# Kernel tuning notes

Measured on AMD Instinct MI355X. Metric: run time of the kernel, lower is better.

Reference implementation:

```python
import jax, jax.numpy as jnp
import numpy as np


def setup_inputs() -> dict:
    key = jax.random.key(0)
    ks = jax.random.split(key, 6)
    B, S, I, H = 8, 4096, 512, 512
    scale = 1.0 / np.sqrt(I)
    return {
        "x": jax.random.normal(ks[0], (B, S, I), dtype=jnp.float32),
        "h_0": jax.random.normal(ks[1], (B, H), dtype=jnp.float32),
        "W_z": jax.random.normal(ks[2], (H, I), dtype=jnp.float32) * scale,
        "b_z": jax.random.normal(ks[3], (H,), dtype=jnp.float32) * scale,
        "W_h": jax.random.normal(ks[4], (H, I), dtype=jnp.float32) * scale,
        "b_h": jax.random.normal(ks[5], (H,), dtype=jnp.float32) * scale,
    }


def reference(x, h_0, W_z, b_z, W_h, b_h):
    # Gate and candidate projections (dense GEMMs over all timesteps at once)
    z = jax.nn.sigmoid(jnp.einsum("bsi,hi->bsh", x, W_z) + b_z)  # [B,S,H]
    h_tilde = jnp.einsum("bsi,hi->bsh", x, W_h) + b_h            # [B,S,H]

    # Linear recurrence h_t = a_t * h_{t-1} + b_t with a = 1-z, b = z*h_tilde.
    # Parallel associative scan over time; h_0 folded in as element 0 (a=1, b=h_0).
    a = jnp.concatenate([jnp.ones_like(h_0)[:, None, :], 1.0 - z], axis=1)     # [B,S+1,H]
    b = jnp.concatenate([h_0[:, None, :], z * h_tilde], axis=1)                # [B,S+1,H]

    def combine(c1, c2):
        a1, b1 = c1
        a2, b2 = c2
        return a1 * a2, a2 * b1 + b2

    _, h = jax.lax.associative_scan(combine, (a, b), axis=1)
    return h[:, 1:, :]  # drop the h_0 slot -> [B,S,H]
```

## Files before the change

kernel.cpp:

```cpp
#include <hip/hip_runtime.h>
#include <hip/hip_bf16.h>
#include <stdint.h>


typedef __attribute__((ext_vector_type(8))) short short8;
typedef __attribute__((ext_vector_type(4))) float f32x4;

#define AS1 __attribute__((address_space(1)))
#define AS3 __attribute__((address_space(3)))

__device__ inline void gload_lds16(const void* g, void* l) {
  __builtin_amdgcn_global_load_lds((AS1 uint32_t*)(g), (AS3 uint32_t*)(l), 16, 0, 0);
}

__device__ inline ushort f2bf(float f) {
  union { __hip_bfloat16 h; ushort u; } v;
  v.h = __float2bfloat16(f);
  return v.u;
}

__global__ void cvt_all(const float* __restrict__ x,
                        const float* __restrict__ wz,
                        const float* __restrict__ wh,
                        ushort* __restrict__ xb,
                        ushort* __restrict__ wzb,
                        ushort* __restrict__ whb) {
  int i = blockIdx.x * 256 + threadIdx.x;
  for (; i < 4325376; i += 2048 * 256) {
    const float* s; ushort* d; int j;
    if (i < 4194304)      { s = x;  d = xb;  j = i; }
    else if (i < 4259840) { s = wz; d = wzb; j = i - 4194304; }
    else                  { s = wh; d = whb; j = i - 4259840; }
    float4 v = reinterpret_cast<const float4*>(s)[j];
    ushort4 o = make_ushort4(f2bf(v.x), f2bf(v.y), f2bf(v.z), f2bf(v.w));
    reinterpret_cast<ushort4*>(d)[j] = o;
  }
}

__global__ __launch_bounds__(256, 2) void gemm_gate(
    const ushort* __restrict__ xb,
    const ushort* __restrict__ wzb,
    const ushort* __restrict__ whb,
    const float* __restrict__ b_z,
    const float* __restrict__ b_h,
    uint* __restrict__ ab,
    float2* __restrict__ ABc)
{
  __shared__ __align__(16) char smem[73728];

  const int t  = threadIdx.x;
  const int w  = t >> 6;
  const int l  = t & 63;
  const int lm = l & 15;
  const int lk = l >> 4;
  const int wm = w >> 1, wn = w & 1;
  const int bid  = blockIdx.x;
  const int tile = (bid & 7) * 128 + (bid >> 3);
  const int bx = tile >> 2;
  const int by = tile & 3;
  const int m0 = bx * 128;
  const int n0 = by * 128;

  const int srow = t >> 2;
  const int ssl  = t & 3;

  f32x4 acc[2][4][4];
  #pragma unroll
  for (int q = 0; q < 2; ++q)
    #pragma unroll
    for (int m = 0; m < 4; ++m)
      #pragma unroll
      for (int n = 0; n < 4; ++n)
        acc[q][m][n] = (f32x4){0.f, 0.f, 0.f, 0.f};

  auto stage = [&](int sel, int kt) {
    char* base = smem + sel * 24576;
    const int k0 = kt * 32;
    #pragma unroll
    for (int j = 0; j < 2; ++j) {
      int row = j * 64 + srow;
      int gs  = ssl ^ ((row >> 1) & 3);
      gload_lds16(xb + (size_t)(m0 + row) * 512 + k0 + gs * 8,
                  base + j * 4096 + w * 1024);
      gload_lds16(wzb + (size_t)(n0 + row) * 512 + k0 + gs * 8,
                  base + 8192 + j * 4096 + w * 1024);
      gload_lds16(whb + (size_t)(n0 + row) * 512 + k0 + gs * 8,
                  base + 16384 + j * 4096 + w * 1024);
    }
  };

  stage(0, 0);
  stage(1, 1);

  #pragma unroll
  for (int kt = 0; kt < 16; ++kt) {
    const int sel = kt % 3;
    if (kt < 14) {
      stage((kt + 2) % 3, kt + 2);
      asm volatile("s_waitcnt vmcnt(12)" ::: "memory");
    } else if (kt == 14) {
      asm volatile("s_waitcnt vmcnt(6)" ::: "memory");
    } else {
      asm volatile("s_waitcnt vmcnt(0)" ::: "memory");
    }
    __builtin_amdgcn_s_barrier();

    const char* base = smem + sel * 24576;
    short8 af[4], bfz[4], bfh[4];
    #pragma unroll
    for (int m = 0; m < 4; ++m) {
      int row = wm * 64 + m * 16 + lm;
      af[m] = *(const short8*)(base + row * 64 + ((lk ^ ((row >> 1) & 3)) << 4));
    }
    #pragma unroll
    for (int n = 0; n < 4; ++n) {
      int row = wn * 64 + n * 16 + lm;
      int so  = ((lk ^ ((row >> 1) & 3)) << 4);
      bfz[n] = *(const short8*)(base + 8192  + row * 64 + so);
      bfh[n] = *(const short8*)(base + 16384 + row * 64 + so);
    }
    __builtin_amdgcn_s_setprio(1);
    #pragma unroll
    for (int m = 0; m < 4; ++m)
      #pragma unroll
      for (int n = 0; n < 4; ++n) {
        acc[0][m][n] = __builtin_amdgcn_mfma_f32_16x16x32_bf16(af[m], bfz[n], acc[0][m][n], 0, 0, 0);
        acc[1][m][n] = __builtin_amdgcn_mfma_f32_16x16x32_bf16(af[m], bfh[n], acc[1][m][n], 0, 0, 0);
      }
    __builtin_amdgcn_s_setprio(0);
    __builtin_amdgcn_s_barrier();
  }

  #pragma unroll
  for (int n = 0; n < 4; ++n) {
    const int col = n0 + wn * 64 + n * 16 + lm;
    const float bzn = b_z[col];
    const float bhn = b_h[col];
    float av[4][4], bv[4][4];
    #pragma unroll
    for (int m = 0; m < 4; ++m) {
      #pragma unroll
      for (int j = 0; j < 4; ++j) {
        size_t grow = (size_t)(m0 + wm * 64 + m * 16 + lk * 4 + j);
        float uz = acc[0][m][n][j] + bzn;
        float uh = acc[1][m][n][j] + bhn;
        float z  = 1.f / (1.f + __expf(-uz));
        float a  = 1.f - z;
        float bb = z * uh;
        av[m][j] = a;
        bv[m][j] = bb;
        ab[grow * 512 + n0 + wn * 64 + n * 16 + lm] =
            (uint)f2bf(a) | ((uint)f2bf(bb) << 16);
      }
    }
    #pragma unroll
    for (int cb = 0; cb < 2; ++cb) {
      float At[2], Bt[2];
      #pragma unroll
      for (int mm = 0; mm < 2; ++mm) {
        float A = 1.f, Bv = 0.f;
        #pragma unroll
        for (int j = 0; j < 4; ++j) {
          float a = av[2 * cb + mm][j];
          float b = bv[2 * cb + mm][j];
          A  = a * A;
          Bv = a * Bv + b;
        }
        float Ag = 1.f, Bg = 0.f;
        #pragma unroll
        for (int q = 0; q < 4; ++q) {
          float Aq = __shfl(A,  lm + 16 * q);
          float Bq = __shfl(Bv, lm + 16 * q);
          Ag = Aq * Ag;
          Bg = Aq * Bg + Bq;
        }
        At[mm] = Ag;
        Bt[mm] = Bg;
      }
      float Achunk = At[1] * At[0];
      float Bchunk = At[1] * Bt[0] + Bt[1];
      if (lk == 0) {
        int bidx = bx >> 5;
        int c    = (bx & 31) * 4 + wm * 2 + cb;
        ABc[((size_t)bidx * 512 + col) * 128 + c] = make_float2(Achunk, Bchunk);
      }
    }
  }
}

__global__ __launch_bounds__(256) void chunk_scan(
    const float2* __restrict__ ABc,
    const float* __restrict__ h0,
    float* __restrict__ Hinit)
{
  __shared__ float sm[128][4];
  const int w = threadIdx.x >> 6, l = threadIdx.x & 63;
  const int b   = blockIdx.x >> 7;
  const int h0g = (blockIdx.x & 127) * 4;
  const int h   = h0g + w;

  const float2* base = ABc + ((size_t)b * 512 + h) * 128;
  float2 s1 = base[l];
  float2 s2 = base[64 + l];

  float A1 = s1.x, B1 = s1.y;
  #pragma unroll
  for (int d = 1; d < 64; d <<= 1) {
    float uA = __shfl_up(A1, d);
    float uB = __shfl_up(B1, d);
    if (l >= d) { B1 = A1 * uB + B1; A1 = A1 * uA; }
  }
  float A2 = s2.x, B2 = s2.y;
  #pragma unroll
  for (int d = 1; d < 64; d <<= 1) {
    float uA = __shfl_up(A2, d);
    float uB = __shfl_up(B2, d);
    if (l >= d) { B2 = A2 * uB + B2; A2 = A2 * uA; }
  }
  float PA = __shfl(A1, 63), PB = __shfl(B1, 63);
  float FA = A2 * PA;
  float FB = A2 * PB + B2;

  float e1A = __shfl_up(A1, 1), e1B = __shfl_up(B1, 1);
  if (l == 0) { e1A = 1.f; e1B = 0.f; }
  float e2A = __shfl_up(FA, 1), e2B = __shfl_up(FB, 1);
  if (l == 0) { e2A = PA; e2B = PB; }

  float h0v = h0[b * 512 + h];
  sm[l][w]      = e1A * h0v + e1B;
  sm[64 + l][w] = e2A * h0v + e2B;
  __syncthreads();

  const int tt = threadIdx.x;
  if (tt < 128) {
    float4 v = *(const float4*)sm[tt];
    *(float4*)(Hinit + ((size_t)b * 128 + tt) * 512 + h0g) = v;
  }
}

__global__ __launch_bounds__(256) void scan_write(
    const uint* __restrict__ ab,
    const float* __restrict__ Hinit,
    float* __restrict__ out)
{
  int tid = blockIdx.x * 256 + threadIdx.x;
  int cg = tid & 127;
  int c  = (tid >> 7) & 127;
  int b  = tid >> 14;
  const uint4* p = reinterpret_cast<const uint4*>(ab + ((size_t)(b * 4096 + c * 32)) * 512) + cg;
  float4 hv = *reinterpret_cast<const float4*>(Hinit + ((size_t)b * 128 + c) * 512 + cg * 4);
  float4* po = reinterpret_cast<float4*>(out + ((size_t)(b * 4096 + c * 32)) * 512) + cg;
  #pragma unroll 4
  for (int t = 0; t < 32; ++t) {
    uint4 u = p[(size_t)t * 128];
    hv.x = __uint_as_float(u.x << 16) * hv.x + __uint_as_float(u.x & 0xffff0000u);
    hv.y = __uint_as_float(u.y << 16) * hv.y + __uint_as_float(u.y & 0xffff0000u);
    hv.z = __uint_as_float(u.z << 16) * hv.z + __uint_as_float(u.z & 0xffff0000u);
    hv.w = __uint_as_float(u.w << 16) * hv.w + __uint_as_float(u.w & 0xffff0000u);
    po[(size_t)t * 128] = hv;
  }
}

extern "C" void kernel_launch(void* const* d_in, const int* in_sizes, int n_in,
                              void* d_out, int out_size, void* d_ws, size_t ws_size,
                              hipStream_t stream) {
  const float* x   = (const float*)d_in[0];
  const float* h0  = (const float*)d_in[1];
  const float* W_z = (const float*)d_in[2];
  const float* b_z = (const float*)d_in[3];
  const float* W_h = (const float*)d_in[4];
  const float* b_h = (const float*)d_in[5];
  float* out = (float*)d_out;

  char* ws = (char*)d_ws;
  ushort* xb    = (ushort*)(ws);
  ushort* wzb   = (ushort*)(ws + 33554432);
  ushort* whb   = (ushort*)(ws + 34078720);
  uint*   ab    = (uint*)  (ws + 34603008);
  float2* ABc   = (float2*)(ws + 101711872);
  float*  Hinit = (float*) (ws + 105906176);

  cvt_all<<<2048, 256, 0, stream>>>(x, W_z, W_h, xb, wzb, whb);
  gemm_gate<<<1024, 256, 0, stream>>>(xb, wzb, whb, b_z, b_h, ab, ABc);
  chunk_scan<<<1024, 256, 0, stream>>>(ABc, h0, Hinit);
  scan_write<<<512, 256, 0, stream>>>(ab, Hinit, out);
}
```

Measured before the change: 94.55 us.

## Fuse fp32-to-bf16 conversion of x into GEMM LDS staging

Drops the separate pass that converted the whole x tensor to bf16 in workspace. The GEMM now streams fp32 x straight into LDS and converts each fragment to bf16 in registers before the MFMAs. Only the weights are still converted up front. This saves a full read and write of x (64 MB fp32 in, 32 MB bf16 out), but doubles x's LDS footprint, so the pipeline drops from triple to double buffering and conversion ALU work lands on the GEMM critical path.

Result: faster. 88.03 us (-6.9%).

```diff
diff --git a/kernel.cpp b/kernel.cpp
--- a/kernel.cpp
+++ b/kernel.cpp
@@ -19,26 +19,19 @@
   return v.u;
 }
 
-__global__ void cvt_all(const float* __restrict__ x,
-                        const float* __restrict__ wz,
-                        const float* __restrict__ wh,
-                        ushort* __restrict__ xb,
-                        ushort* __restrict__ wzb,
-                        ushort* __restrict__ whb) {
+__global__ void cvt_w(const float* __restrict__ wz, const float* __restrict__ wh,
+                      ushort* __restrict__ wzb, ushort* __restrict__ whb) {
   int i = blockIdx.x * 256 + threadIdx.x;
-  for (; i < 4325376; i += 2048 * 256) {
-    const float* s; ushort* d; int j;
-    if (i < 4194304)      { s = x;  d = xb;  j = i; }
-    else if (i < 4259840) { s = wz; d = wzb; j = i - 4194304; }
-    else                  { s = wh; d = whb; j = i - 4259840; }
-    float4 v = reinterpret_cast<const float4*>(s)[j];
-    ushort4 o = make_ushort4(f2bf(v.x), f2bf(v.y), f2bf(v.z), f2bf(v.w));
-    reinterpret_cast<ushort4*>(d)[j] = o;
-  }
+  float4 a = reinterpret_cast<const float4*>(wz)[i];
+  reinterpret_cast<ushort4*>(wzb)[i] =
+      make_ushort4(f2bf(a.x), f2bf(a.y), f2bf(a.z), f2bf(a.w));
+  float4 b = reinterpret_cast<const float4*>(wh)[i];
+  reinterpret_cast<ushort4*>(whb)[i] =
+      make_ushort4(f2bf(b.x), f2bf(b.y), f2bf(b.z), f2bf(b.w));
 }
 
 __global__ __launch_bounds__(256, 2) void gemm_gate(
-    const ushort* __restrict__ xb,
+    const float* __restrict__ x,
     const ushort* __restrict__ wzb,
     const ushort* __restrict__ whb,
     const float* __restrict__ b_z,
@@ -46,7 +39,7 @@
     uint* __restrict__ ab,
     float2* __restrict__ ABc)
 {
-  __shared__ __align__(16) char smem[73728];
+  __shared__ __align__(16) char smem[65536];
 
   const int t  = threadIdx.x;
   const int w  = t >> 6;
@@ -74,50 +67,58 @@
         acc[q][m][n] = (f32x4){0.f, 0.f, 0.f, 0.f};
 
   auto stage = [&](int sel, int kt) {
-    char* base = smem + sel * 24576;
+    char* base = smem + sel * 32768;
     const int k0 = kt * 32;
     #pragma unroll
     for (int j = 0; j < 2; ++j) {
-      int row = j * 64 + srow;
-      int gs  = ssl ^ ((row >> 1) & 3);
-      gload_lds16(xb + (size_t)(m0 + row) * 512 + k0 + gs * 8,
-                  base + j * 4096 + w * 1024);
+      int row  = j * 64 + srow;
+      int sw   = (row >> 1) & 3;
+      int qlog = ssl ^ sw;
+      const float* xs = x + (size_t)(m0 + row) * 512 + k0 + qlog * 8;
+      gload_lds16(xs,     base +        j * 4096 + w * 1024);
+      gload_lds16(xs + 4, base + 8192 + j * 4096 + w * 1024);
+      int gs = ssl ^ sw;
       gload_lds16(wzb + (size_t)(n0 + row) * 512 + k0 + gs * 8,
-                  base + 8192 + j * 4096 + w * 1024);
+                  base + 16384 + j * 4096 + w * 1024);
       gload_lds16(whb + (size_t)(n0 + row) * 512 + k0 + gs * 8,
-                  base + 16384 + j * 4096 + w * 1024);
+                  base + 24576 + j * 4096 + w * 1024);
     }
   };
 
   stage(0, 0);
-  stage(1, 1);
 
   #pragma unroll
   for (int kt = 0; kt < 16; ++kt) {
-    const int sel = kt % 3;
-    if (kt < 14) {
-      stage((kt + 2) % 3, kt + 2);
-      asm volatile("s_waitcnt vmcnt(12)" ::: "memory");
-    } else if (kt == 14) {
-      asm volatile("s_waitcnt vmcnt(6)" ::: "memory");
+    const int sel = kt & 1;
+    if (kt < 15) {
+      stage(sel ^ 1, kt + 1);
+      asm volatile("s_waitcnt vmcnt(8)" ::: "memory");
     } else {
       asm volatile("s_waitcnt vmcnt(0)" ::: "memory");
     }
     __builtin_amdgcn_s_barrier();
 
-    const char* base = smem + sel * 24576;
+    const char* base = smem + sel * 32768;
     short8 af[4], bfz[4], bfh[4];
     #pragma unroll
     for (int m = 0; m < 4; ++m) {
       int row = wm * 64 + m * 16 + lm;
-      af[m] = *(const short8*)(base + row * 64 + ((lk ^ ((row >> 1) & 3)) << 4));
+      int so  = ((lk ^ ((row >> 1) & 3)) << 4);
+      f32x4 lo = *(const f32x4*)(base +        row * 64 + so);
+      f32x4 hi = *(const f32x4*)(base + 8192 + row * 64 + so);
+      short8 v;
+      v[0] = (short)f2bf(lo[0]); v[1] = (short)f2bf(lo[1]);
+      v[2] = (short)f2bf(lo[2]); v[3] = (short)f2bf(lo[3]);
+      v[4] = (short)f2bf(hi[0]); v[5] = (short)f2bf(hi[1]);
+      v[6] = (short)f2bf(hi[2]); v[7] = (short)f2bf(hi[3]);
+      af[m] = v;
     }
     #pragma unroll
     for (int n = 0; n < 4; ++n) {
       int row = wn * 64 + n * 16 + lm;
       int so  = ((lk ^ ((row >> 1) & 3)) << 4);
-      bfz[n] = *(const short8*)(base + 8192  + row * 64 + so);
-      bfh[n] = *(const short8*)(base + 16384 + row * 64 + so);
+      bfz[n] = *(const short8*)(base + 16384 + row * 64 + so);
+      bfh[n] = *(const short8*)(base + 24576 + row * 64 + so);
     }
     __builtin_amdgcn_s_setprio(1);
     #pragma unroll
@@ -149,8 +150,7 @@
         float bb = z * uh;
         av[m][j] = a;
         bv[m][j] = bb;
-        ab[grow * 512 + n0 + wn * 64 + n * 16 + lm] =
-            (uint)f2bf(a) | ((uint)f2bf(bb) << 16);
+        ab[grow * 512 + col] = (uint)f2bf(a) | ((uint)f2bf(bb) << 16);
       }
     }
     #pragma unroll
@@ -273,15 +273,14 @@
   float* out = (float*)d_out;
 
   char* ws = (char*)d_ws;
-  ushort* xb    = (ushort*)(ws);
-  ushort* wzb   = (ushort*)(ws + 33554432);
-  ushort* whb   = (ushort*)(ws + 34078720);
-  uint*   ab    = (uint*)  (ws + 34603008);
-  float2* ABc   = (float2*)(ws + 101711872);
-  float*  Hinit = (float*) (ws + 105906176);
-
-  cvt_all<<<2048, 256, 0, stream>>>(x, W_z, W_h, xb, wzb, whb);
-  gemm_gate<<<1024, 256, 0, stream>>>(xb, wzb, whb, b_z, b_h, ab, ABc);
+  ushort* wzb   = (ushort*)(ws);
+  ushort* whb   = (ushort*)(ws + 524288);
+  uint*   ab    = (uint*)  (ws + 1048576);
+  float2* ABc   = (float2*)(ws + 68157440);
+  float*  Hinit = (float*) (ws + 72351744);
+
+  cvt_w<<<256, 256, 0, stream>>>(W_z, W_h, wzb, whb);
+  gemm_gate<<<1024, 256, 0, stream>>>(x, wzb, whb, b_z, b_h, ab, ABc);
   chunk_scan<<<1024, 256, 0, stream>>>(ABc, h0, Hinit);
   scan_write<<<512, 256, 0, stream>>>(ab, Hinit, out);
 }
```
